# Performance work log

Hardware: AMD Instinct MI355X
Metric: run time of the kernel (lower is better)

## Reference

```python
import jax, jax.numpy as jnp
import numpy as np

B, P, H, W = 8, 128, 32, 32
NC = 4                 # num_classes = NUM_REL_GROUP + 1
DOBJ = 4424            # 2*DOBJ = 8848
CIN = 256
C = 128 + 8848         # 8976 GCN channel dim


def setup_inputs() -> dict:
    key = jax.random.key(0)
    ks = jax.random.split(key, 24)
    s = 0.02  # weight scale to keep activations moderate
    inp = {
        "x": jax.random.normal(ks[0], (B, CIN, H, W), jnp.float32),
        "rel_pair_idxs": jax.random.randint(ks[1], (B, P, 2), 0, 640, dtype=jnp.int32),
        "obj_rep": jax.random.normal(ks[2], (640, DOBJ), jnp.float32),
        # ADD_GCN params
        "fc_w": jax.random.normal(ks[3], (NC, CIN), jnp.float32) * s,
        "ct_w": jax.random.normal(ks[4], (128, CIN), jnp.float32) * s,
        "ct_b": jnp.zeros((128,), jnp.float32),
        # DynamicGraphConvolution params
        "A": jax.random.normal(ks[5], (NC, NC), jnp.float32) * 0.25,          # static_adj conv1d (no bias)
        "sw_w": jax.random.normal(ks[6], (C, C), jnp.float32) * s / np.sqrt(C) * 30,
        "sw_b": jnp.zeros((C,), jnp.float32),
        "cg_w": jax.random.normal(ks[7], (C, C), jnp.float32) * s / np.sqrt(C) * 30,
        "cg_b": jnp.zeros((C,), jnp.float32),
        "bn_g": jnp.ones((C,), jnp.float32),
        "bn_b": jnp.zeros((C,), jnp.float32),
        "bn_m": jnp.zeros((C,), jnp.float32),
        "bn_v": jnp.ones((C,), jnp.float32),
        "co_w": jax.random.normal(ks[8], (NC, 2 * C), jnp.float32) * s / np.sqrt(C) * 30,
        "co_b": jnp.zeros((NC,), jnp.float32),
        "dw_w": jax.random.normal(ks[9], (C, C), jnp.float32) * s / np.sqrt(C) * 30,
        "dw_b": jnp.zeros((C,), jnp.float32),
        "ll_w": jax.random.normal(ks[10], (NC, C), jnp.float32) * s / np.sqrt(C) * 30,
        "ll_b": jnp.zeros((NC,), jnp.float32),
        "mask_mat": jnp.eye(NC, dtype=jnp.float32),
    }
    return inp


def reference(x, rel_pair_idxs, obj_rep, fc_w, ct_w, ct_b, A, sw_w, sw_b,
              cg_w, cg_b, bn_g, bn_b, bn_m, bn_v, co_w, co_b, dw_w, dw_b,
              ll_w, ll_b, mask_mat):
    leaky = lambda t: jax.nn.leaky_relu(t, 0.2)
    b, cin, h, w = x.shape
    xr = x.reshape(b, cin, h * w)                                  # (B,256,HW)

    # forward_classification_sm: fc -> topk(1).mean == max over spatial
    y = jnp.einsum('oc,bcs->bos', fc_w, xr)                        # (B,NC,HW)
    out1 = y.max(-1)                                               # (B,NC)

    # forward_sam
    mask = jax.nn.sigmoid(y)                                       # (B,NC,HW)
    v = jnp.einsum('oc,bcs->bos', ct_w, xr) + ct_b[None, :, None]  # (B,128,HW)
    v = jnp.einsum('bcs,bns->bcn', v, mask)                        # (B,128,NC)

    # pairwise object features (gather), tiled over NC node slots
    o1 = obj_rep[rel_pair_idxs[..., 0]]                            # (B,P,DOBJ)
    o2 = obj_rep[rel_pair_idxs[..., 1]]
    pf = jnp.concatenate([o1, o2], -1)                             # (B,P,8848)
    p = pf.shape[1]
    pf = jnp.broadcast_to(pf[..., None], pf.shape + (NC,))         # (B,P,8848,NC)
    vb = jnp.broadcast_to(v[:, None], (b, p) + v.shape[1:])        # (B,P,128,NC)
    g = jnp.concatenate([pf, vb], 2).reshape(b * p, C, NC)         # (BP,C,NC)

    # --- DynamicGraphConvolution ---
    # static GCN: node-mix conv1d (no bias) + leaky, then channel 1x1 conv + leaky
    xs = leaky(jnp.einsum('nm,pcm->pcn', A, g))                    # (BP,C,NC)
    xs = leaky(jnp.einsum('oc,pcn->pon', sw_w, xs) + sw_b[None, :, None])
    hg = g + xs

    # dynamic adjacency
    glb = hg.mean(-1)                                              # (BP,C) gap
    glb = glb @ cg_w.T + cg_b                                      # conv_global (1x1)
    glb = (glb - bn_m) * jax.lax.rsqrt(bn_v + 1e-5) * bn_g + bn_b  # BN (eval)
    glb = leaky(glb)
    # conv_create_co_mat over cat([glb_expand, hg], ch) without materializing cat
    adj = jax.nn.sigmoid(
        jnp.einsum('oc,pc->po', co_w[:, :C], glb)[:, :, None]
        + jnp.einsum('oc,pcn->pon', co_w[:, C:], hg)
        + co_b[None, :, None])                                     # (BP,NC,NC)

    # dynamic GCN
    hd = leaky(jnp.einsum('pcn,pnm->pcm', hg, adj))
    z = leaky(jnp.einsum('oc,pcn->pon', dw_w, hd) + dw_b[None, :, None])  # (BP,C,NC)

    # head: last_linear + leaky, masked diagonal sum
    out2 = leaky(jnp.einsum('oc,pcn->pon', ll_w, z) + ll_b[None, :, None])  # (BP,NC,NC)
    out2 = (out2 * jax.lax.stop_gradient(mask_mat)).sum(-1)        # (BP,NC)

    o1b = jnp.broadcast_to(out1[:, None], (b, p, NC)).reshape(b * p, NC)
    return ((o1b + out2) * 0.5).reshape(b, p, NC)
```

## Files before the change

kernel.cpp:

```cpp
#include <hip/hip_runtime.h>
#include <stdint.h>

#define DEVI __device__ __forceinline__

typedef unsigned short u16;
typedef __bf16 bf16x8 __attribute__((ext_vector_type(8)));
typedef float f32x4 __attribute__((ext_vector_type(4)));
typedef u16 u16x8 __attribute__((ext_vector_type(8)));

DEVI u16 f2bf(float f){
  union { float f; unsigned u; } v; v.f = f;
  unsigned r = v.u + 0x7FFFu + ((v.u >> 16) & 1u);
  return (u16)(r >> 16);
}
DEVI float bf2f(u16 h){
  union { unsigned u; float f; } v; v.u = ((unsigned)h) << 16;
  return v.f;
}
DEVI float lky(float t){ return t > 0.f ? t : 0.2f * t; }

#define GLD16(gp, lp) __builtin_amdgcn_global_load_lds( \
    (const __attribute__((address_space(1))) void*)(gp), \
    (__attribute__((address_space(3))) void*)(lp), 16, 0, 0)


DEVI void stage_half(const u16* __restrict__ G, size_t grow0, int kcol, int Kp,
                     u16* lds, int t)
{
  #pragma unroll
  for (int j = 0; j < 2; ++j){
    const int off16 = j*512 + t;
    const int rl = off16 >> 3, sl = off16 & 7;
    const u16* gp = G + (grow0 + rl)*(size_t)Kp + kcol + ((sl ^ (rl & 7))*8);
    GLD16(gp, lds + off16*8);
  }
}

template<int RB, int RA>
DEVI void ph_reads(const u16* __restrict__ Ab, const u16* __restrict__ Bb,
                   bf16x8 (&afr)[4][2], bf16x8 (&bfr)[4][2],
                   int wr, int wc, int l4, int l15)
{
  if constexpr (RA >= 0){
    #pragma unroll
    for (int m = 0; m < 4; ++m){
      const int r = wr*128 + RA*64 + m*16 + l15;
      afr[m][0] = *(const bf16x8*)&Ab[r*64 + (((0+l4) ^ (r & 7))*8)];
      afr[m][1] = *(const bf16x8*)&Ab[r*64 + (((4+l4) ^ (r & 7))*8)];
    }
  }
  if constexpr (RB >= 0){
    #pragma unroll
    for (int nn = 0; nn < 2; ++nn){
      const int r = wc*64 + (RB+nn)*16 + l15;
      bfr[RB+nn][0] = *(const bf16x8*)&Bb[r*64 + (((0+l4) ^ (r & 7))*8)];
      bfr[RB+nn][1] = *(const bf16x8*)&Bb[r*64 + (((4+l4) ^ (r & 7))*8)];
    }
  }
}

template<int MH, int NH, int VM>
DEVI void ph_mfma(bf16x8 (&afr)[4][2], bf16x8 (&bfr)[4][2], f32x4 (&acc)[8][4])
{
  __builtin_amdgcn_s_barrier();
  asm volatile("s_waitcnt lgkmcnt(0)" ::: "memory");
  __builtin_amdgcn_sched_barrier(0);
  __builtin_amdgcn_s_setprio(1);
  #pragma unroll
  for (int m = 0; m < 4; ++m)
    #pragma unroll
    for (int nn = 0; nn < 2; ++nn)
      #pragma unroll
      for (int ks = 0; ks < 2; ++ks)
        acc[MH*4+m][NH+nn] = __builtin_amdgcn_mfma_f32_16x16x32_bf16(
            afr[m][ks], bfr[NH+nn][ks], acc[MH*4+m][NH+nn], 0, 0, 0);
  __builtin_amdgcn_s_setprio(0);
  if constexpr (VM == 4){
    __builtin_amdgcn_sched_barrier(0);
    asm volatile("s_waitcnt vmcnt(4)" ::: "memory");
  }
  __builtin_amdgcn_s_barrier();
}

template<int EPI>
__global__ __launch_bounds__(512, 2)
void gemm256(const u16* __restrict__ A, const u16* __restrict__ B,
             int Kp, int Nt, int Mreal, float* __restrict__ C, long long ldc,
             const float* __restrict__ bias, const float* __restrict__ scale,
             const float* __restrict__ off, const float* __restrict__ llw,
             float* __restrict__ oacc)
{
  __shared__ __align__(16) u16 As[2][16384];
  __shared__ __align__(16) u16 Bs[2][16384];
  const int t    = threadIdx.x;
  const int lane = t & 63;
  const int wid  = t >> 6;
  const int wr = wid >> 2, wc = wid & 3;
  const int l4 = lane >> 4, l15 = lane & 15;

  const int nwg = gridDim.x;
  const int xc = blockIdx.x & 7, pp = blockIdx.x >> 3;
  const int qq = nwg >> 3, rr = nwg & 7;
  const int wg = (xc < rr ? xc*(qq+1) : rr*(qq+1) + (xc-rr)*qq) + pp;
  const int mt = wg / Nt, nt = wg % Nt;

  const size_t am0 = (size_t)mt*256;
  const size_t bn0 = (size_t)nt*256;

  f32x4 acc[8][4];
  #pragma unroll
  for (int i = 0; i < 8; ++i)
    #pragma unroll
    for (int j = 0; j < 4; ++j) acc[i][j] = f32x4{0.f,0.f,0.f,0.f};
  bf16x8 afr[4][2], bfr[4][2];

  const int NT2 = Kp >> 6;
  const int NI  = NT2 >> 1;

  stage_half(A, am0+0,   0,  Kp, &As[0][0],    t);
  stage_half(A, am0+128, 0,  Kp, &As[0][8192], t);
  stage_half(B, bn0+0,   0,  Kp, &Bs[0][0],    t);
  stage_half(B, bn0+128, 0,  Kp, &Bs[0][8192], t);
  stage_half(B, bn0+0,   64, Kp, &Bs[1][0],    t);
  stage_half(B, bn0+128, 64, Kp, &Bs[1][8192], t);
  asm volatile("s_waitcnt vmcnt(4)" ::: "memory");
  __builtin_amdgcn_s_barrier();

  for (int i = 0; i < NI; ++i){
    const int k1  = 2*i + 1;
    const int ts0 = (2*i+2 < NT2) ? 2*i+2 : 2*i;
    const int ts1 = (2*i+3 < NT2) ? 2*i+3 : 2*i+1;
    ph_reads<0,0>(&As[0][0], &Bs[0][0], afr, bfr, wr, wc, l4, l15);
    stage_half(A, am0+0,   k1*64,  Kp, &As[1][0],    t);
    ph_mfma<0,0,-1>(afr, bfr, acc);
    ph_reads<2,-1>(&As[0][0], &Bs[0][0], afr, bfr, wr, wc, l4, l15);
    stage_half(A, am0+128, k1*64,  Kp, &As[1][8192], t);
    ph_mfma<0,2,-1>(afr, bfr, acc);
    ph_reads<-1,1>(&As[0][0], &Bs[0][0], afr, bfr, wr, wc, l4, l15);
    stage_half(B, bn0+0,   ts0*64, Kp, &Bs[0][0],    t);
    ph_mfma<1,2,-1>(afr, bfr, acc);
    stage_half(B, bn0+128, ts0*64, Kp, &Bs[0][8192], t);
    ph_mfma<1,0,4>(afr, bfr, acc);
    ph_reads<0,0>(&As[1][0], &Bs[1][0], afr, bfr, wr, wc, l4, l15);
    stage_half(A, am0+0,   ts0*64, Kp, &As[0][0],    t);
    ph_mfma<0,0,-1>(afr, bfr, acc);
    ph_reads<2,-1>(&As[1][0], &Bs[1][0], afr, bfr, wr, wc, l4, l15);
    stage_half(A, am0+128, ts0*64, Kp, &As[0][8192], t);
    ph_mfma<0,2,-1>(afr, bfr, acc);
    ph_reads<-1,1>(&As[1][0], &Bs[1][0], afr, bfr, wr, wc, l4, l15);
    stage_half(B, bn0+0,   ts1*64, Kp, &Bs[1][0],    t);
    ph_mfma<1,2,-1>(afr, bfr, acc);
    stage_half(B, bn0+128, ts1*64, Kp, &Bs[1][8192], t);
    ph_mfma<1,0,4>(afr, bfr, acc);
  }
  asm volatile("s_waitcnt vmcnt(0)" ::: "memory");

  const int ob0 = mt*256 + wr*128;
  const int nb0 = nt*256 + wc*64;

  if (EPI == 0){
    #pragma unroll
    for (int mi = 0; mi < 8; ++mi){
      const int ob = ob0 + mi*16 + l4*4;
      if (ob < Mreal){
        #pragma unroll
        for (int ni = 0; ni < 4; ++ni){
          const int n = nb0 + ni*16 + l15;
          *(f32x4*)&C[(size_t)n*ldc + ob] = acc[mi][ni];
        }
      }
    }
  } else if (EPI == 2){
    #pragma unroll
    for (int mi = 0; mi < 8; ++mi){
      const int ob = ob0 + mi*16 + l4*4;
      if (ob < Mreal){
        const float sc0=scale[ob],sc1=scale[ob+1],sc2=scale[ob+2],sc3=scale[ob+3];
        const float of0=off[ob],of1=off[ob+1],of2=off[ob+2],of3=off[ob+3];
        #pragma unroll
        for (int ni = 0; ni < 4; ++ni){
          const int n = nb0 + ni*16 + l15;
          f32x4 a = acc[mi][ni];
          f32x4 vv = { lky(a[0]*sc0+of0), lky(a[1]*sc1+of1),
                       lky(a[2]*sc2+of2), lky(a[3]*sc3+of3) };
          *(f32x4*)&C[(size_t)n*ldc + ob] = vv;
        }
      }
    }
  } else {
    #pragma unroll
    for (int ni = 0; ni < 4; ++ni){
      float s0=0.f, s1=0.f, s2=0.f, s3=0.f;
      #pragma unroll
      for (int mi = 0; mi < 8; ++mi){
        #pragma unroll
        for (int r = 0; r < 4; ++r){
          const int o = ob0 + mi*16 + l4*4 + r;
          if (o < Mreal){
            const float val = lky(acc[mi][ni][r] + bias[o]);
            s0 += llw[o]         * val;
            s1 += llw[8976 + o]  * val;
            s2 += llw[17952 + o] * val;
            s3 += llw[26928 + o] * val;
          }
        }
      }
      const int n = nb0 + ni*16 + l15;
      const int q = n >> 2, m = n & 3;
      float sv[4] = {s0,s1,s2,s3};
      #pragma unroll
      for (int o4 = 0; o4 < 4; ++o4){
        float tt = sv[o4];
        tt += __shfl_xor(tt, 16);
        tt += __shfl_xor(tt, 32);
        if (l4 == 0) atomicAdd(&oacc[(q*4 + o4)*4 + m], tt);
      }
    }
  }
}

template<int EPI>
__global__ __launch_bounds__(256)
void gemm_bf16(const u16* __restrict__ A, const u16* __restrict__ B,
               int Kp, int Nt, int Mreal, float* __restrict__ C, long long ldc,
               const float* __restrict__ bias)
{
  __shared__ __align__(16) u16 As[2][4096];
  __shared__ __align__(16) u16 Bs[2][4096];
  const int tid  = threadIdx.x;
  const int lane = tid & 63;
  const int wr   = (tid >> 6) >> 1, wc = (tid >> 6) & 1;
  const int l4   = lane >> 4, l15 = lane & 15;
  const int mt   = blockIdx.x / Nt, nt = blockIdx.x % Nt;

  const size_t arow = (size_t)(mt*128 + (tid>>2)) * Kp + (tid&3)*8;
  const size_t brow = (size_t)(nt*128 + (tid>>2)) * Kp + (tid&3)*8;
  const int    ldst = (tid>>2)*32 + (tid&3)*8;
  const size_t rowskip = (size_t)64 * Kp;

  f32x4 acc[4][4];
  #pragma unroll
  for (int i=0;i<4;i++)
    #pragma unroll
    for (int j=0;j<4;j++) acc[i][j] = f32x4{0.f,0.f,0.f,0.f};

  const int NT = Kp >> 5;
  {
    const u16* a0 = A + arow; const u16* b0 = B + brow;
    GLD16(a0,           &As[0][ldst]);
    GLD16(a0 + rowskip, &As[0][ldst + 2048]);
    GLD16(b0,           &Bs[0][ldst]);
    GLD16(b0 + rowskip, &Bs[0][ldst + 2048]);
  }
  __syncthreads();

  for (int kt=0; kt<NT; ++kt){
    const int cur = kt & 1;
    if (kt + 1 < NT){
      const u16* a0 = A + arow + (size_t)(kt+1)*32;
      const u16* b0 = B + brow + (size_t)(kt+1)*32;
      GLD16(a0,           &As[cur^1][ldst]);
      GLD16(a0 + rowskip, &As[cur^1][ldst + 2048]);
      GLD16(b0,           &Bs[cur^1][ldst]);
      GLD16(b0 + rowskip, &Bs[cur^1][ldst + 2048]);
    }
    bf16x8 af[4], bf[4];
    #pragma unroll
    for (int mi=0;mi<4;mi++)
      af[mi] = *(const bf16x8*)&As[cur][(wr*64 + mi*16 + l15)*32 + l4*8];
    #pragma unroll
    for (int ni=0;ni<4;ni++)
      bf[ni] = *(const bf16x8*)&Bs[cur][(wc*64 + ni*16 + l15)*32 + l4*8];
    #pragma unroll
    for (int mi=0;mi<4;mi++)
      #pragma unroll
      for (int ni=0;ni<4;ni++)
        acc[mi][ni] = __builtin_amdgcn_mfma_f32_16x16x32_bf16(af[mi], bf[ni], acc[mi][ni], 0, 0, 0);
    __syncthreads();
  }

  const int ob0 = mt*128 + wr*64;
  const int nb0 = nt*128 + wc*64;
  #pragma unroll
  for (int mi=0;mi<4;mi++)
    #pragma unroll
    for (int r=0;r<4;r++){
      const int o = ob0 + mi*16 + l4*4 + r;
      if (o < Mreal){
        const float bb = bias[o];
        #pragma unroll
        for (int ni=0;ni<4;ni++){
          const int n = nb0 + ni*16 + l15;
          C[(size_t)o*ldc + n] = acc[mi][ni][r] + bb;
        }
      }
    }
}

__global__ void k_cvt_pad(const float* __restrict__ src, int srows, int scols,
                          int lds_, int koff, u16* __restrict__ dst, int Kp)
{
  const int r = blockIdx.x;
  const int nch = Kp >> 3;
  for (int ch = threadIdx.x; ch < nch; ch += blockDim.x){
    const int k = ch*8;
    u16 o[8];
    if (r < srows){
      #pragma unroll
      for (int i=0;i<8;i++){
        const int kk = k + i;
        o[i] = (kk < scols) ? f2bf(src[(size_t)r*lds_ + koff + kk]) : (u16)0;
      }
    } else {
      #pragma unroll
      for (int i=0;i<8;i++) o[i] = 0;
    }
    u16x8 vv = { o[0],o[1],o[2],o[3],o[4],o[5],o[6],o[7] };
    *(u16x8*)&dst[(size_t)r*Kp + k] = vv;
  }
}

__global__ void k_cvt_obj(const float* __restrict__ obj, u16* __restrict__ dst)
{
  const int r = blockIdx.x;
  const int ab = (r >= 640);
  const float* src = obj + (size_t)(ab ? r-640 : r)*4424;
  for (int ch = threadIdx.x; ch < 560; ch += 256){
    const int k = ch*8;
    u16 o[8];
    #pragma unroll
    for (int i=0;i<8;i++){
      const int kk = k+i;
      float f = (kk < 4424) ? src[kk] : 0.f;
      if (ab) f = fabsf(f);
      o[i] = f2bf(f);
    }
    u16x8 vv = { o[0],o[1],o[2],o[3],o[4],o[5],o[6],o[7] };
    *(u16x8*)&dst[(size_t)r*4480 + k] = vv;
  }
}

__global__ void k_combine(const float* __restrict__ U, const int* __restrict__ rel,
                          float* __restrict__ P12)
{
  const int q = blockIdx.x;
  const int i1 = rel[q*2], i2 = rel[q*2+1];
  const float* u1  = U + (size_t)i1*17952;
  const float* u2  = U + (size_t)i2*17952 + 8976;
  const float* u1a = U + (size_t)(640+i1)*17952;
  const float* u2a = U + (size_t)(640+i2)*17952 + 8976;
  float* p1 = P12 + (size_t)q*8976;
  float* p2 = P12 + (size_t)(1024+q)*8976;
  for (int c = threadIdx.x*4; c < 8976; c += 1024){
    f32x4 a  = *(const f32x4*)&u1[c];
    f32x4 b  = *(const f32x4*)&u2[c];
    f32x4 aa = *(const f32x4*)&u1a[c];
    f32x4 bb = *(const f32x4*)&u2a[c];
    *(f32x4*)&p1[c] = a + b;
    *(f32x4*)&p2[c] = aa + bb;
  }
}

__global__ void k_xT(const float* __restrict__ x, u16* __restrict__ xT)
{
  __shared__ float t[32][33];
  const int bid = blockIdx.x;
  const int b = bid >> 8; const int cs = (bid >> 5) & 7; const int ss = bid & 31;
  const int tx = threadIdx.x & 31, ty = threadIdx.x >> 5;
  #pragma unroll
  for (int i=0;i<4;i++){
    const int r = ty + i*8;
    t[r][tx] = x[((size_t)(b*256 + cs*32 + r))*1024 + ss*32 + tx];
  }
  __syncthreads();
  #pragma unroll
  for (int i=0;i<4;i++){
    const int r = ty + i*8;
    xT[((size_t)(b*1024 + ss*32 + r))*256 + cs*32 + tx] = f2bf(t[tx][r]);
  }
}

__global__ void k_ymask(const float* __restrict__ x, const float* __restrict__ fcw,
                        float* __restrict__ y, float* __restrict__ mask)
{
  __shared__ float fc[1024];
  const int b = blockIdx.x >> 2, st = blockIdx.x & 3;
  for (int i=threadIdx.x; i<1024; i+=256) fc[i] = fcw[i];
  __syncthreads();
  const int s = st*256 + threadIdx.x;
  float a0=0,a1=0,a2=0,a3=0;
  for (int c=0;c<256;c++){
    const float xv = x[((size_t)(b*256+c))*1024 + s];
    a0 += fc[c]*xv; a1 += fc[256+c]*xv; a2 += fc[512+c]*xv; a3 += fc[768+c]*xv;
  }
  const size_t base = (size_t)(b*4)*1024 + s;
  y[base]        = a0; mask[base]        = 1.f/(1.f+expf(-a0));
  y[base+1024]   = a1; mask[base+1024]   = 1.f/(1.f+expf(-a1));
  y[base+2048]   = a2; mask[base+2048]   = 1.f/(1.f+expf(-a2));
  y[base+3072]   = a3; mask[base+3072]   = 1.f/(1.f+expf(-a3));
}

__global__ void k_out1(const float* __restrict__ y, float* __restrict__ out1){
  const int bn = blockIdx.x;
  float m = -3.4e38f;
  for (int s=threadIdx.x; s<1024; s+=256) m = fmaxf(m, y[(size_t)bn*1024+s]);
  for (int o=32;o;o>>=1) m = fmaxf(m, __shfl_xor(m,o));
  __shared__ float red[4];
  if ((threadIdx.x&63)==0) red[threadIdx.x>>6] = m;
  __syncthreads();
  if (threadIdx.x==0) out1[bn] = fmaxf(fmaxf(red[0],red[1]),fmaxf(red[2],red[3]));
}

__global__ void k_v(const float* __restrict__ vpreT, const float* __restrict__ mask,
                    float* __restrict__ v){
  const int b = blockIdx.x >> 7, j = blockIdx.x & 127;
  float a[4]={0,0,0,0};
  for (int s=threadIdx.x; s<1024; s+=256){
    const float pv = vpreT[(size_t)j*8192 + b*1024 + s];
    #pragma unroll
    for (int m=0;m<4;m++) a[m] += pv * mask[((size_t)(b*4+m))*1024 + s];
  }
  __shared__ float red[4][5];
  #pragma unroll
  for (int m=0;m<4;m++){
    float t=a[m];
    for (int o=32;o;o>>=1) t += __shfl_xor(t,o);
    if ((threadIdx.x&63)==0) red[m][threadIdx.x>>6]=t;
  }
  __syncthreads();
  if (threadIdx.x<4)
    v[(size_t)(b*128+j)*4 + threadIdx.x] =
      red[threadIdx.x][0]+red[threadIdx.x][1]+red[threadIdx.x][2]+red[threadIdx.x][3];
}

__global__ void k_lv(const float* __restrict__ Am, const float* __restrict__ v,
                     float* __restrict__ lv){
  const int idx = blockIdx.x*256 + threadIdx.x;
  if (idx < 1024){
    #pragma unroll
    for (int n=0;n<4;n++){
      float s=0;
      #pragma unroll
      for (int m=0;m<4;m++) s += Am[n*4+m]*v[idx*4+m];
      lv[idx*4+n] = lky(s);
    }
  }
}

__global__ void k_sV(const float* __restrict__ sw, const float* __restrict__ lv,
                     float* __restrict__ sV){
  __shared__ float l[4096];
  for (int i=threadIdx.x; i<4096; i+=256) l[i]=lv[i];
  __syncthreads();
  const int o = blockIdx.x*256 + threadIdx.x;
  if (o >= 8976) return;
  float acc[8][4] = {};
  const float* row = sw + (size_t)o*8976 + 8848;
  for (int j=0;j<128;j++){
    const float wv = row[j];
    #pragma unroll
    for (int b=0;b<8;b++){
      const float* lb = &l[(b*128+j)*4];
      #pragma unroll
      for (int n=0;n<4;n++) acc[b][n] += wv*lb[n];
    }
  }
  #pragma unroll
  for (int b=0;b<8;b++){
    f32x4 vv = {acc[b][0],acc[b][1],acc[b][2],acc[b][3]};
    *(f32x4*)&sV[((size_t)b*8976 + o)*4] = vv;
  }
}

__global__ void k_so(const float* __restrict__ cgb, const float* __restrict__ g,
                     const float* __restrict__ b2, const float* __restrict__ m,
                     const float* __restrict__ vvar, float* __restrict__ so){
  const int o = blockIdx.x*256+threadIdx.x;
  if (o<8976){
    const float sc = g[o]*rsqrtf(vvar[o]+1e-5f);
    so[o]=sc; so[8976+o] = (cgb[o]-m[o])*sc + b2[o];
  }
}

__global__ void k_glb_t2(const float* __restrict__ P12, const float* __restrict__ obj,
                         const int* __restrict__ rel,
                         const float* __restrict__ sV, const float* __restrict__ swb,
                         const float* __restrict__ v, const float* __restrict__ Am,
                         const float* __restrict__ cow, u16* __restrict__ glbB,
                         float* __restrict__ t2)
{
  const int q = blockIdx.x; const int b = q >> 7;
  const int i1 = rel[q*2], i2 = rel[q*2+1];
  const float* o1 = obj + (size_t)i1*4424;
  const float* o2 = obj + (size_t)i2*4424;
  float rA[4], aA[4];
  #pragma unroll
  for (int n=0;n<4;n++){
    const float s = Am[n*4]+Am[n*4+1]+Am[n*4+2]+Am[n*4+3];
    rA[n]=0.6f*s; aA[n]=0.4f*fabsf(s);
  }
  float t2a[16] = {};
  for (int c = threadIdx.x; c < 9216; c += 256){
    if (c < 8976){
      const float p1 = P12[(size_t)q*8976 + c];
      const float p2 = P12[(size_t)(1024+q)*8976 + c];
      const f32x4 sv = *(const f32x4*)&sV[((size_t)b*8976 + c)*4];
      const float sb = swb[c];
      const float gs = (c < 4424) ? o1[c] : (c < 8848) ? o2[c-4424] : 0.f;
      float hg[4]; float sum = 0.f;
      #pragma unroll
      for (int n=0;n<4;n++){
        const float xs2 = lky(rA[n]*p1 + aA[n]*p2 + sv[n] + sb);
        const float g = (c < 8848) ? gs : v[((size_t)b*128 + (c-8848))*4 + n];
        hg[n] = g + xs2; sum += hg[n];
      }
      glbB[(size_t)q*9216 + c] = f2bf(0.25f*sum);
      #pragma unroll
      for (int o4=0;o4<4;o4++){
        const float cw = cow[(size_t)o4*17952 + 8976 + c];
        #pragma unroll
        for (int n=0;n<4;n++) t2a[o4*4+n] += cw*hg[n];
      }
    } else {
      glbB[(size_t)q*9216 + c] = 0;
    }
  }
  __shared__ float red[16][5];
  #pragma unroll
  for (int i=0;i<16;i++){
    float t = t2a[i];
    for (int o=32;o;o>>=1) t += __shfl_xor(t,o);
    if ((threadIdx.x&63)==0) red[i][threadIdx.x>>6]=t;
  }
  __syncthreads();
  if (threadIdx.x < 16)
    t2[q*16+threadIdx.x] = red[threadIdx.x][0]+red[threadIdx.x][1]
                          +red[threadIdx.x][2]+red[threadIdx.x][3];
}

__global__ void k_adj(const float* __restrict__ glb2, const float* __restrict__ cow,
                      const float* __restrict__ t2, const float* __restrict__ cob,
                      float* __restrict__ adj)
{
  const int q = blockIdx.x;
  float a[4]={0,0,0,0};
  for (int c=threadIdx.x; c<8976; c+=256){
    const float g = glb2[(size_t)q*8976+c];
    #pragma unroll
    for (int o=0;o<4;o++) a[o] += cow[(size_t)o*17952 + c]*g;
  }
  __shared__ float red[4][5]; __shared__ float co1[4];
  #pragma unroll
  for (int i=0;i<4;i++){
    float t=a[i]; for (int o=32;o;o>>=1) t += __shfl_xor(t,o);
    if ((threadIdx.x&63)==0) red[i][threadIdx.x>>6]=t;
  }
  __syncthreads();
  if (threadIdx.x<4)
    co1[threadIdx.x]=red[threadIdx.x][0]+red[threadIdx.x][1]+red[threadIdx.x][2]+red[threadIdx.x][3];
  __syncthreads();
  if (threadIdx.x<16){
    const int a_=threadIdx.x>>2, m=threadIdx.x&3;
    const float t = co1[a_] + t2[q*16 + a_*4 + m] + cob[a_];
    adj[q*16 + a_*4 + m] = 1.f/(1.f+expf(-t));
  }
}

__global__ void k_hd(const float* __restrict__ P12, const float* __restrict__ obj,
                     const int* __restrict__ rel,
                     const float* __restrict__ sV, const float* __restrict__ swb,
                     const float* __restrict__ v, const float* __restrict__ Am,
                     const float* __restrict__ adj, u16* __restrict__ hdb)
{
  const int q = blockIdx.x; const int b = q>>7;
  const int i1 = rel[q*2], i2 = rel[q*2+1];
  const float* o1 = obj + (size_t)i1*4424;
  const float* o2 = obj + (size_t)i2*4424;
  float rA[4], aA[4];
  #pragma unroll
  for (int n=0;n<4;n++){
    const float s = Am[n*4]+Am[n*4+1]+Am[n*4+2]+Am[n*4+3];
    rA[n]=0.6f*s; aA[n]=0.4f*fabsf(s);
  }
  __shared__ float aj[16];
  if (threadIdx.x<16) aj[threadIdx.x] = adj[q*16+threadIdx.x];
  __syncthreads();
  float ajr[16];
  #pragma unroll
  for (int i=0;i<16;i++) ajr[i]=aj[i];
  for (int c=threadIdx.x; c<9216; c+=256){
    if (c<8976){
      const float p1 = P12[(size_t)q*8976 + c];
      const float p2 = P12[(size_t)(1024+q)*8976 + c];
      const f32x4 sv = *(const f32x4*)&sV[((size_t)b*8976 + c)*4];
      const float sb = swb[c];
      const float gs = (c < 4424) ? o1[c] : (c < 8848) ? o2[c-4424] : 0.f;
      float hg[4];
      #pragma unroll
      for (int n=0;n<4;n++){
        const float xs2 = lky(rA[n]*p1 + aA[n]*p2 + sv[n] + sb);
        const float g = (c < 8848) ? gs : v[((size_t)b*128 + (c-8848))*4 + n];
        hg[n] = g + xs2;
      }
      #pragma unroll
      for (int m=0;m<4;m++){
        const float hv = lky(hg[0]*ajr[m] + hg[1]*ajr[4+m] + hg[2]*ajr[8+m] + hg[3]*ajr[12+m]);
        hdb[((size_t)(q*4+m))*9216 + c] = f2bf(hv);
      }
    } else {
      #pragma unroll
      for (int m=0;m<4;m++) hdb[((size_t)(q*4+m))*9216 + c] = 0;
    }
  }
}

__global__ void k_final(const float* __restrict__ o2f, const float* __restrict__ out1,
                        const float* __restrict__ llb, const float* __restrict__ mm,
                        float* __restrict__ out)
{
  const int idx = blockIdx.x*256+threadIdx.x;
  if (idx < 4096){
    const int q = idx>>2, o = idx&3, b = q>>7;
    float s=0.f;
    #pragma unroll
    for (int m=0;m<4;m++) s += lky(o2f[(q*4+o)*4+m] + llb[o]) * mm[o*4+m];
    out[idx] = 0.5f*(out1[b*4+o] + s);
  }
}

extern "C" void kernel_launch(void* const* d_in, const int* in_sizes, int n_in,
                              void* d_out, int out_size, void* d_ws, size_t ws_size,
                              hipStream_t stream)
{
  const float* x    = (const float*)d_in[0];
  const int*   rel  = (const int*)d_in[1];
  const float* obj  = (const float*)d_in[2];
  const float* fcw  = (const float*)d_in[3];
  const float* ctw  = (const float*)d_in[4];
  const float* ctb  = (const float*)d_in[5];
  const float* Am   = (const float*)d_in[6];
  const float* sww  = (const float*)d_in[7];
  const float* swb  = (const float*)d_in[8];
  const float* cgw  = (const float*)d_in[9];
  const float* cgb  = (const float*)d_in[10];
  const float* bng  = (const float*)d_in[11];
  const float* bnb  = (const float*)d_in[12];
  const float* bnm  = (const float*)d_in[13];
  const float* bnv  = (const float*)d_in[14];
  const float* cow  = (const float*)d_in[15];
  const float* cob  = (const float*)d_in[16];
  const float* dww  = (const float*)d_in[17];
  const float* dwb  = (const float*)d_in[18];
  const float* llw  = (const float*)d_in[19];
  const float* llb  = (const float*)d_in[20];
  const float* mm   = (const float*)d_in[21];
  float* out = (float*)d_out;
  (void)in_sizes; (void)n_in; (void)out_size; (void)ws_size;

  char* ws = (char*)d_ws;
  size_t off = 0;
  auto alloc = [&](size_t bytes)->char*{
    char* p = ws + off; off = (off + bytes + 255) & ~(size_t)255; return p;
  };
  u16*   Wb    = (u16*)  alloc((size_t)9216*9216*2);
  char*  UG    = alloc((size_t)94371840);
  float* U     = (float*)UG;
  u16*   glbB  = (u16*)  UG;
  u16*   hdb   = (u16*)  (UG + (size_t)18874368);
  u16*   objB  = (u16*)  alloc((size_t)1280*4480*2);
  float* P12   = (float*)alloc((size_t)2048*8976*4);
  float* glb2  = (float*)alloc((size_t)1024*8976*4);
  u16*   xT    = (u16*)  alloc((size_t)8192*256*2);
  u16*   ctwb  = (u16*)  alloc((size_t)128*256*2);
  float* y     = (float*)alloc((size_t)32768*4);
  float* mask  = (float*)alloc((size_t)32768*4);
  float* out1  = (float*)alloc((size_t)32*4);
  float* vpreT = (float*)alloc((size_t)128*8192*4);
  float* v     = (float*)alloc((size_t)4096*4);
  float* lv    = (float*)alloc((size_t)4096*4);
  float* sV    = (float*)alloc((size_t)287232*4);
  float* so    = (float*)alloc((size_t)2*8976*4);
  float* t2    = (float*)alloc((size_t)16384*4);
  float* adj   = (float*)alloc((size_t)16384*4);
  float* o2f   = (float*)alloc((size_t)16384*4);

  k_xT<<<dim3(2048), dim3(256), 0, stream>>>(x, xT);
  k_cvt_pad<<<dim3(128), dim3(256), 0, stream>>>(ctw, 128, 256, 256, 0, ctwb, 256);
  k_ymask<<<dim3(32), dim3(256), 0, stream>>>(x, fcw, y, mask);
  k_out1<<<dim3(32), dim3(256), 0, stream>>>(y, out1);
  gemm_bf16<1><<<dim3(64), dim3(256), 0, stream>>>(
      ctwb, xT, 256, 64, 128, vpreT, (long long)8192, ctb);
  k_v<<<dim3(1024), dim3(256), 0, stream>>>(vpreT, mask, v);

  k_cvt_obj<<<dim3(1280), dim3(256), 0, stream>>>(obj, objB);
  k_cvt_pad<<<dim3(8976), dim3(256), 0, stream>>>(sww, 8976, 4424, 8976, 0, Wb, 4480);
  k_cvt_pad<<<dim3(9200), dim3(256), 0, stream>>>(sww, 8976, 4424, 8976, 4424,
                                                  Wb + (size_t)8976*4480, 4480);
  gemm256<0><<<dim3(71*5), dim3(512), 0, stream>>>(
      Wb, objB, 4480, 5, 17952, U, (long long)17952,
      nullptr, nullptr, nullptr, nullptr, nullptr);
  k_combine<<<dim3(1024), dim3(256), 0, stream>>>(U, rel, P12);

  k_lv<<<dim3(4), dim3(256), 0, stream>>>(Am, v, lv);
  k_sV<<<dim3(36), dim3(256), 0, stream>>>(sww, lv, sV);
  k_glb_t2<<<dim3(1024), dim3(256), 0, stream>>>(P12, obj, rel, sV, swb, v, Am,
                                                 cow, glbB, t2);

  k_cvt_pad<<<dim3(9216), dim3(256), 0, stream>>>(cgw, 8976, 8976, 8976, 0, Wb, 9216);
  k_so<<<dim3(36), dim3(256), 0, stream>>>(cgb, bng, bnb, bnm, bnv, so);
  gemm256<2><<<dim3(36*4), dim3(512), 0, stream>>>(
      Wb, glbB, 9216, 4, 8976, glb2, (long long)8976,
      nullptr, so, so + 8976, nullptr, nullptr);

  k_adj<<<dim3(1024), dim3(256), 0, stream>>>(glb2, cow, t2, cob, adj);
  k_cvt_pad<<<dim3(9216), dim3(256), 0, stream>>>(dww, 8976, 8976, 8976, 0, Wb, 9216);
  k_hd<<<dim3(1024), dim3(256), 0, stream>>>(P12, obj, rel, sV, swb, v, Am, adj, hdb);

  hipMemsetAsync(o2f, 0, (size_t)16384*4, stream);
  gemm256<3><<<dim3(36*16), dim3(512), 0, stream>>>(
      Wb, hdb, 9216, 16, 8976, nullptr, 0, dwb,
      nullptr, nullptr, llw, o2f);

  k_final<<<dim3(16), dim3(256), 0, stream>>>(o2f, out1, llb, mm, out);
}
```

Baseline: 2.165 ms.

## Fuse fp32-to-bf16 weight conversion into GEMM A-operand loads

Removes the separate k_cvt_pad passes that wrote the large weight matrices to a bf16 workspace. The GEMM now loads fp32 weights directly into registers, converts them to bf16 and writes them into swizzled LDS inside the pipelined main loop, with bounds masking and stacked-row handling for the sw_w split. The K padding for the glb and hd operands shrinks from 9216 to 9088. This trades a full extra read and write of each weight matrix for more register pressure, conversion ALU work inside the loop and a more complex wait and barrier schedule.

```diff
diff --git a/kernel.cpp b/kernel.cpp
--- a/kernel.cpp
+++ b/kernel.cpp
@@ -7,6 +7,7 @@
 typedef __bf16 bf16x8 __attribute__((ext_vector_type(8)));
 typedef float f32x4 __attribute__((ext_vector_type(4)));
 typedef u16 u16x8 __attribute__((ext_vector_type(8)));
+typedef u16 u16x4 __attribute__((ext_vector_type(4)));
 
 DEVI u16 f2bf(float f){
   union { float f; unsigned u; } v; v.f = f;
@@ -24,43 +25,8 @@
     (__attribute__((address_space(3))) void*)(lp), 16, 0, 0)
 
 
-DEVI void stage_half(const u16* __restrict__ G, size_t grow0, int kcol, int Kp,
-                     u16* lds, int t)
-{
-  #pragma unroll
-  for (int j = 0; j < 2; ++j){
-    const int off16 = j*512 + t;
-    const int rl = off16 >> 3, sl = off16 & 7;
-    const u16* gp = G + (grow0 + rl)*(size_t)Kp + kcol + ((sl ^ (rl & 7))*8);
-    GLD16(gp, lds + off16*8);
-  }
-}
-
-template<int RB, int RA>
-DEVI void ph_reads(const u16* __restrict__ Ab, const u16* __restrict__ Bb,
-                   bf16x8 (&afr)[4][2], bf16x8 (&bfr)[4][2],
-                   int wr, int wc, int l4, int l15)
-{
-  if constexpr (RA >= 0){
-    #pragma unroll
-    for (int m = 0; m < 4; ++m){
-      const int r = wr*128 + RA*64 + m*16 + l15;
-      afr[m][0] = *(const bf16x8*)&Ab[r*64 + (((0+l4) ^ (r & 7))*8)];
-      afr[m][1] = *(const bf16x8*)&Ab[r*64 + (((4+l4) ^ (r & 7))*8)];
-    }
-  }
-  if constexpr (RB >= 0){
-    #pragma unroll
-    for (int nn = 0; nn < 2; ++nn){
-      const int r = wc*64 + (RB+nn)*16 + l15;
-      bfr[RB+nn][0] = *(const bf16x8*)&Bb[r*64 + (((0+l4) ^ (r & 7))*8)];
-      bfr[RB+nn][1] = *(const bf16x8*)&Bb[r*64 + (((4+l4) ^ (r & 7))*8)];
-    }
-  }
-}
-
-template<int MH, int NH, int VM>
-DEVI void ph_mfma(bf16x8 (&afr)[4][2], bf16x8 (&bfr)[4][2], f32x4 (&acc)[8][4])
+template<int VM>
+DEVI void PH(bf16x8 (&afr)[4], bf16x8 (&bfr)[4], f32x4 (&acc)[8][4], int H)
 {
   __builtin_amdgcn_s_barrier();
   asm volatile("s_waitcnt lgkmcnt(0)" ::: "memory");
@@ -69,26 +35,28 @@
   #pragma unroll
   for (int m = 0; m < 4; ++m)
     #pragma unroll
-    for (int nn = 0; nn < 2; ++nn)
-      #pragma unroll
-      for (int ks = 0; ks < 2; ++ks)
-        acc[MH*4+m][NH+nn] = __builtin_amdgcn_mfma_f32_16x16x32_bf16(
-            afr[m][ks], bfr[NH+nn][ks], acc[MH*4+m][NH+nn], 0, 0, 0);
+    for (int n = 0; n < 4; ++n)
+      acc[H*4+m][n] = __builtin_amdgcn_mfma_f32_16x16x32_bf16(
+          afr[m], bfr[n], acc[H*4+m][n], 0, 0, 0);
   __builtin_amdgcn_s_setprio(0);
-  if constexpr (VM == 4){
+  if constexpr (VM == 10){
     __builtin_amdgcn_sched_barrier(0);
-    asm volatile("s_waitcnt vmcnt(4)" ::: "memory");
+    asm volatile("s_waitcnt vmcnt(10)" ::: "memory");
+  } else if constexpr (VM == 12){
+    __builtin_amdgcn_sched_barrier(0);
+    asm volatile("s_waitcnt vmcnt(12)" ::: "memory");
   }
   __builtin_amdgcn_s_barrier();
 }
 
-template<int EPI>
+template<int EPI, int STACKED>
 __global__ __launch_bounds__(512, 2)
-void gemm256(const u16* __restrict__ A, const u16* __restrict__ B,
-             int Kp, int Nt, int Mreal, float* __restrict__ C, long long ldc,
-             const float* __restrict__ bias, const float* __restrict__ scale,
-             const float* __restrict__ off, const float* __restrict__ llw,
-             float* __restrict__ oacc)
+void gemmF(const float* __restrict__ A, const u16* __restrict__ B,
+           int Astride, int Kreal, int Kp, int Mrows, int Nt, int Mreal,
+           float* __restrict__ C, long long ldc,
+           const float* __restrict__ bias, const float* __restrict__ scale,
+           const float* __restrict__ off, const float* __restrict__ llw,
+           float* __restrict__ oacc)
 {
   __shared__ __align__(16) u16 As[2][16384];
   __shared__ __align__(16) u16 Bs[2][16384];
@@ -104,56 +72,117 @@
   const int wg = (xc < rr ? xc*(qq+1) : rr*(qq+1) + (xc-rr)*qq) + pp;
   const int mt = wg / Nt, nt = wg % Nt;
 
-  const size_t am0 = (size_t)mt*256;
-  const size_t bn0 = (size_t)nt*256;
+  const int am0 = mt*256;
+  const int bn0 = nt*256;
 
   f32x4 acc[8][4];
   #pragma unroll
   for (int i = 0; i < 8; ++i)
     #pragma unroll
     for (int j = 0; j < 4; ++j) acc[i][j] = f32x4{0.f,0.f,0.f,0.f};
-  bf16x8 afr[4][2], bfr[4][2];
+  bf16x8 afr[4], bfr[4];
+  f32x4 ra[8];
 
   const int NT2 = Kp >> 6;
   const int NI  = NT2 >> 1;
 
-  stage_half(A, am0+0,   0,  Kp, &As[0][0],    t);
-  stage_half(A, am0+128, 0,  Kp, &As[0][8192], t);
-  stage_half(B, bn0+0,   0,  Kp, &Bs[0][0],    t);
-  stage_half(B, bn0+128, 0,  Kp, &Bs[0][8192], t);
-  stage_half(B, bn0+0,   64, Kp, &Bs[1][0],    t);
-  stage_half(B, bn0+128, 64, Kp, &Bs[1][8192], t);
-  asm volatile("s_waitcnt vmcnt(4)" ::: "memory");
+  auto BSTAGE = [&](int tile, int buf, int h){
+    const int kc = tile*64;
+    u16* lbase = (buf ? &Bs[1][0] : &Bs[0][0]) + h*8192;
+    #pragma unroll
+    for (int j = 0; j < 2; ++j){
+      const int u = j*512 + t;
+      const int rl = u >> 3, sl = u & 7;
+      const u16* gp = B + (size_t)(bn0 + h*128 + rl)*Kp + kc + ((sl ^ (rl & 7))*8);
+      GLD16(gp, lbase + u*8);
+    }
+  };
+  auto ALOAD = [&](int tile){
+    const int kc = tile*64;
+    #pragma unroll
+    for (int j = 0; j < 8; ++j){
+      const int h = j >> 2;
+      const int u = (j & 3)*512 + t;
+      const int row = am0 + h*128 + (u >> 4);
+      const int col = kc + (u & 15)*4;
+      int ro = row, ko = 0;
+      if (STACKED){ if (row >= 8976){ ro = row - 8976; ko = 4424; } }
+      const bool ok = (row < Mrows) && (col < Kreal);
+      const float* p = A + (size_t)(ok ? ro : 0)*Astride + ko + (ok ? col : 0);
+      f32x4 v = __builtin_nontemporal_load((const f32x4*)p);
+      ra[j] = ok ? v : f32x4{0.f,0.f,0.f,0.f};
+    }
+  };
+  auto AWRITE_H = [&](int buf, int h){
+    u16* lb = buf ? &As[1][0] : &As[0][0];
+    #pragma unroll
+    for (int jj = 0; jj < 4; ++jj){
+      const int j = h*4 + jj;
+      const int u = jj*512 + t;
+      const int rl = h*128 + (u >> 4);
+      const int cu = u & 15, koct = cu >> 1, hu = cu & 1;
+      f32x4 v = ra[j];
+      u16x4 w = { f2bf(v[0]), f2bf(v[1]), f2bf(v[2]), f2bf(v[3]) };
+      *(u16x4*)&lb[rl*64 + ((koct ^ (rl & 7))*8) + hu*4] = w;
+    }
+  };
+  auto RDA = [&](int buf, int h, int ks){
+    const u16* lb = buf ? &As[1][0] : &As[0][0];
+    #pragma unroll
+    for (int m = 0; m < 4; ++m){
+      const int r = wr*128 + h*64 + m*16 + l15;
+      afr[m] = *(const bf16x8*)&lb[r*64 + (((ks*4 + l4) ^ (r & 7))*8)];
+    }
+  };
+  auto RDB = [&](int buf, int ks){
+    const u16* lb = buf ? &Bs[1][0] : &Bs[0][0];
+    #pragma unroll
+    for (int n = 0; n < 4; ++n){
+      const int r = wc*64 + n*16 + l15;
+      bfr[n] = *(const bf16x8*)&lb[r*64 + (((ks*4 + l4) ^ (r & 7))*8)];
+    }
+  };
+  #define FENCE asm volatile("" ::: "memory")
+
+  ALOAD(0);                 FENCE;
+  BSTAGE(0,0,0); BSTAGE(0,0,1);  FENCE;
+  AWRITE_H(0,0); AWRITE_H(0,1);  FENCE;
+  BSTAGE(1,1,0); BSTAGE(1,1,1);  FENCE;
+  ALOAD(1);                 FENCE;
+  asm volatile("s_waitcnt vmcnt(12)" ::: "memory");
+  asm volatile("s_waitcnt lgkmcnt(0)" ::: "memory");
   __builtin_amdgcn_s_barrier();
 
   for (int i = 0; i < NI; ++i){
-    const int k1  = 2*i + 1;
-    const int ts0 = (2*i+2 < NT2) ? 2*i+2 : 2*i;
-    const int ts1 = (2*i+3 < NT2) ? 2*i+3 : 2*i+1;
-    ph_reads<0,0>(&As[0][0], &Bs[0][0], afr, bfr, wr, wc, l4, l15);
-    stage_half(A, am0+0,   k1*64,  Kp, &As[1][0],    t);
-    ph_mfma<0,0,-1>(afr, bfr, acc);
-    ph_reads<2,-1>(&As[0][0], &Bs[0][0], afr, bfr, wr, wc, l4, l15);
-    stage_half(A, am0+128, k1*64,  Kp, &As[1][8192], t);
-    ph_mfma<0,2,-1>(afr, bfr, acc);
-    ph_reads<-1,1>(&As[0][0], &Bs[0][0], afr, bfr, wr, wc, l4, l15);
-    stage_half(B, bn0+0,   ts0*64, Kp, &Bs[0][0],    t);
-    ph_mfma<1,2,-1>(afr, bfr, acc);
-    stage_half(B, bn0+128, ts0*64, Kp, &Bs[0][8192], t);
-    ph_mfma<1,0,4>(afr, bfr, acc);
-    ph_reads<0,0>(&As[1][0], &Bs[1][0], afr, bfr, wr, wc, l4, l15);
-    stage_half(A, am0+0,   ts0*64, Kp, &As[0][0],    t);
-    ph_mfma<0,0,-1>(afr, bfr, acc);
-    ph_reads<2,-1>(&As[1][0], &Bs[1][0], afr, bfr, wr, wc, l4, l15);
-    stage_half(A, am0+128, ts0*64, Kp, &As[0][8192], t);
-    ph_mfma<0,2,-1>(afr, bfr, acc);
-    ph_reads<-1,1>(&As[1][0], &Bs[1][0], afr, bfr, wr, wc, l4, l15);
-    stage_half(B, bn0+0,   ts1*64, Kp, &Bs[1][0],    t);
-    ph_mfma<1,2,-1>(afr, bfr, acc);
-    stage_half(B, bn0+128, ts1*64, Kp, &Bs[1][8192], t);
-    ph_mfma<1,0,4>(afr, bfr, acc);
-  }
-  asm volatile("s_waitcnt vmcnt(0)" ::: "memory");
+    const int ta = (2*i+2 < NT2) ? 2*i+2 : NT2-1;
+    const int tb = (2*i+3 < NT2) ? 2*i+3 : NT2-1;
+    AWRITE_H(1,0);
+    RDA(0,0,0); RDB(0,0);
+    PH<-1>(afr, bfr, acc, 0);
+    AWRITE_H(1,1);
+    RDA(0,1,0);
+    PH<-1>(afr, bfr, acc, 1);
+    RDA(0,0,1); RDB(0,1);
+    ALOAD(ta);
+    PH<-1>(afr, bfr, acc, 0);
+    RDA(0,1,1);
+    BSTAGE(ta,0,0);
+    PH<10>(afr, bfr, acc, 1);
+    AWRITE_H(0,0);
+    RDA(1,0,0); RDB(1,0);
+    BSTAGE(ta,0,1);
+    PH<-1>(afr, bfr, acc, 0);
+    AWRITE_H(0,1);
+    RDA(1,1,0);
+    PH<-1>(afr, bfr, acc, 1);
+    RDA(1,0,1); RDB(1,1);
+    ALOAD(tb);
+    PH<-1>(afr, bfr, acc, 0);
+    RDA(1,1,1);
+    BSTAGE(tb,1,0); BSTAGE(tb,1,1);
+    PH<12>(afr, bfr, acc, 1);
+  }
+  asm volatile("s_waitcnt vmcnt(0) lgkmcnt(0)" ::: "memory");
 
   const int ob0 = mt*256 + wr*128;
   const int nb0 = nt*256 + wc*64;
@@ -219,9 +248,8 @@
   }
 }
 
-template<int EPI>
 __global__ __launch_bounds__(256)
-void gemm_bf16(const u16* __restrict__ A, const u16* __restrict__ B,
+void gemm_vpre(const u16* __restrict__ A, const u16* __restrict__ B,
                int Kp, int Nt, int Mreal, float* __restrict__ C, long long ldc,
                const float* __restrict__ bias)
 {
@@ -500,7 +528,7 @@
     rA[n]=0.6f*s; aA[n]=0.4f*fabsf(s);
   }
   float t2a[16] = {};
-  for (int c = threadIdx.x; c < 9216; c += 256){
+  for (int c = threadIdx.x; c < 9088; c += 256){
     if (c < 8976){
       const float p1 = P12[(size_t)q*8976 + c];
       const float p2 = P12[(size_t)(1024+q)*8976 + c];
@@ -514,7 +542,7 @@
         const float g = (c < 8848) ? gs : v[((size_t)b*128 + (c-8848))*4 + n];
         hg[n] = g + xs2; sum += hg[n];
       }
-      glbB[(size_t)q*9216 + c] = f2bf(0.25f*sum);
+      glbB[(size_t)q*9088 + c] = f2bf(0.25f*sum);
       #pragma unroll
       for (int o4=0;o4<4;o4++){
         const float cw = cow[(size_t)o4*17952 + 8976 + c];
@@ -522,7 +550,7 @@
         for (int n=0;n<4;n++) t2a[o4*4+n] += cw*hg[n];
       }
     } else {
-      glbB[(size_t)q*9216 + c] = 0;
+      glbB[(size_t)q*9088 + c] = 0;
     }
   }
   __shared__ float red[16][5];
@@ -588,7 +616,7 @@
   float ajr[16];
   #pragma unroll
   for (int i=0;i<16;i++) ajr[i]=aj[i];
-  for (int c=threadIdx.x; c<9216; c+=256){
+  for (int c=threadIdx.x; c<9088; c+=256){
     if (c<8976){
       const float p1 = P12[(size_t)q*8976 + c];
       const float p2 = P12[(size_t)(1024+q)*8976 + c];
@@ -605,11 +633,11 @@
       #pragma unroll
       for (int m=0;m<4;m++){
         const float hv = lky(hg[0]*ajr[m] + hg[1]*ajr[4+m] + hg[2]*ajr[8+m] + hg[3]*ajr[12+m]);
-        hdb[((size_t)(q*4+m))*9216 + c] = f2bf(hv);
+        hdb[((size_t)(q*4+m))*9088 + c] = f2bf(hv);
       }
     } else {
       #pragma unroll
-      for (int m=0;m<4;m++) hdb[((size_t)(q*4+m))*9216 + c] = 0;
+      for (int m=0;m<4;m++) hdb[((size_t)(q*4+m))*9088 + c] = 0;
     }
   }
 }
@@ -662,11 +690,10 @@
   auto alloc = [&](size_t bytes)->char*{
     char* p = ws + off; off = (off + bytes + 255) & ~(size_t)255; return p;
   };
-  u16*   Wb    = (u16*)  alloc((size_t)9216*9216*2);
   char*  UG    = alloc((size_t)94371840);
   float* U     = (float*)UG;
   u16*   glbB  = (u16*)  UG;
-  u16*   hdb   = (u16*)  (UG + (size_t)18874368);
+  u16*   hdb   = (u16*)  (UG + (size_t)1024*9088*2);
   u16*   objB  = (u16*)  alloc((size_t)1280*4480*2);
   float* P12   = (float*)alloc((size_t)2048*8976*4);
   float* glb2  = (float*)alloc((size_t)1024*8976*4);
@@ -688,16 +715,13 @@
   k_cvt_pad<<<dim3(128), dim3(256), 0, stream>>>(ctw, 128, 256, 256, 0, ctwb, 256);
   k_ymask<<<dim3(32), dim3(256), 0, stream>>>(x, fcw, y, mask);
   k_out1<<<dim3(32), dim3(256), 0, stream>>>(y, out1);
-  gemm_bf16<1><<<dim3(64), dim3(256), 0, stream>>>(
+  gemm_vpre<<<dim3(64), dim3(256), 0, stream>>>(
       ctwb, xT, 256, 64, 128, vpreT, (long long)8192, ctb);
   k_v<<<dim3(1024), dim3(256), 0, stream>>>(vpreT, mask, v);
 
   k_cvt_obj<<<dim3(1280), dim3(256), 0, stream>>>(obj, objB);
-  k_cvt_pad<<<dim3(8976), dim3(256), 0, stream>>>(sww, 8976, 4424, 8976, 0, Wb, 4480);
-  k_cvt_pad<<<dim3(9200), dim3(256), 0, stream>>>(sww, 8976, 4424, 8976, 4424,
-                                                  Wb + (size_t)8976*4480, 4480);
-  gemm256<0><<<dim3(71*5), dim3(512), 0, stream>>>(
-      Wb, objB, 4480, 5, 17952, U, (long long)17952,
+  gemmF<0,1><<<dim3(71*5), dim3(512), 0, stream>>>(
+      sww, objB, 8976, 4424, 4480, 17952, 5, 17952, U, (long long)17952,
       nullptr, nullptr, nullptr, nullptr, nullptr);
   k_combine<<<dim3(1024), dim3(256), 0, stream>>>(U, rel, P12);
 
@@ -706,20 +730,18 @@
   k_glb_t2<<<dim3(1024), dim3(256), 0, stream>>>(P12, obj, rel, sV, swb, v, Am,
                                                  cow, glbB, t2);
 
-  k_cvt_pad<<<dim3(9216), dim3(256), 0, stream>>>(cgw, 8976, 8976, 8976, 0, Wb, 9216);
   k_so<<<dim3(36), dim3(256), 0, stream>>>(cgb, bng, bnb, bnm, bnv, so);
-  gemm256<2><<<dim3(36*4), dim3(512), 0, stream>>>(
-      Wb, glbB, 9216, 4, 8976, glb2, (long long)8976,
+  gemmF<2,0><<<dim3(36*4), dim3(512), 0, stream>>>(
+      cgw, glbB, 8976, 8976, 9088, 8976, 4, 8976, glb2, (long long)8976,
       nullptr, so, so + 8976, nullptr, nullptr);
 
   k_adj<<<dim3(1024), dim3(256), 0, stream>>>(glb2, cow, t2, cob, adj);
-  k_cvt_pad<<<dim3(9216), dim3(256), 0, stream>>>(dww, 8976, 8976, 8976, 0, Wb, 9216);
   k_hd<<<dim3(1024), dim3(256), 0, stream>>>(P12, obj, rel, sV, swb, v, Am, adj, hdb);
 
   hipMemsetAsync(o2f, 0, (size_t)16384*4, stream);
-  gemm256<3><<<dim3(36*16), dim3(512), 0, stream>>>(
-      Wb, hdb, 9216, 16, 8976, nullptr, 0, dwb,
-      nullptr, nullptr, llw, o2f);
+  gemmF<3,0><<<dim3(36*16), dim3(512), 0, stream>>>(
+      dww, hdb, 8976, 8976, 9088, 8976, 16, 8976, nullptr, 0,
+      dwb, nullptr, nullptr, llw, o2f);
 
   k_final<<<dim3(16), dim3(256), 0, stream>>>(o2f, out1, llb, mm, out);
 }
```

Result: slower. 4.118 ms (+90.2%).

## Fuse pair-combine into consumers, shrink K padding, add strip tile ordering

Applied to the files above, without the earlier changes.

Removes the k_combine kernel and the P12 intermediate: k_glb_t2 and k_hd now gather the two U rows per pair and add them inline. The K padding for the 8976-dim GEMMs drops from 9216 to 9088, so the weight conversion and the GEMM main loops do less padded work. gemm256 gains an SN parameter that groups N-tiles into strips to improve L2 reuse, and the dw GEMM uses strips of 8. The intent is to cut memory traffic and one launch. In exchange U is read twice with scattered rows, and the 9088 padding must stay compatible with the 128-wide K step.

```diff
diff --git a/kernel.cpp b/kernel.cpp
--- a/kernel.cpp
+++ b/kernel.cpp
@@ -85,7 +85,7 @@
 template<int EPI>
 __global__ __launch_bounds__(512, 2)
 void gemm256(const u16* __restrict__ A, const u16* __restrict__ B,
-             int Kp, int Nt, int Mreal, float* __restrict__ C, long long ldc,
+             int Kp, int Nt, int SN, int Mreal, float* __restrict__ C, long long ldc,
              const float* __restrict__ bias, const float* __restrict__ scale,
              const float* __restrict__ off, const float* __restrict__ llw,
              float* __restrict__ oacc)
@@ -102,7 +102,9 @@
   const int xc = blockIdx.x & 7, pp = blockIdx.x >> 3;
   const int qq = nwg >> 3, rr = nwg & 7;
   const int wg = (xc < rr ? xc*(qq+1) : rr*(qq+1) + (xc-rr)*qq) + pp;
-  const int mt = wg / Nt, nt = wg % Nt;
+  const int strip_sz = (nwg / Nt) * SN;
+  const int strip = wg / strip_sz, srem = wg % strip_sz;
+  const int mt = srem / SN, nt = strip*SN + srem % SN;
 
   const size_t am0 = (size_t)mt*256;
   const size_t bn0 = (size_t)nt*256;
@@ -219,9 +221,8 @@
   }
 }
 
-template<int EPI>
 __global__ __launch_bounds__(256)
-void gemm_bf16(const u16* __restrict__ A, const u16* __restrict__ B,
+void gemm_vpre(const u16* __restrict__ A, const u16* __restrict__ B,
                int Kp, int Nt, int Mreal, float* __restrict__ C, long long ldc,
                const float* __restrict__ bias)
 {
@@ -340,27 +341,6 @@
   }
 }
 
-__global__ void k_combine(const float* __restrict__ U, const int* __restrict__ rel,
-                          float* __restrict__ P12)
-{
-  const int q = blockIdx.x;
-  const int i1 = rel[q*2], i2 = rel[q*2+1];
-  const float* u1  = U + (size_t)i1*17952;
-  const float* u2  = U + (size_t)i2*17952 + 8976;
-  const float* u1a = U + (size_t)(640+i1)*17952;
-  const float* u2a = U + (size_t)(640+i2)*17952 + 8976;
-  float* p1 = P12 + (size_t)q*8976;
-  float* p2 = P12 + (size_t)(1024+q)*8976;
-  for (int c = threadIdx.x*4; c < 8976; c += 1024){
-    f32x4 a  = *(const f32x4*)&u1[c];
-    f32x4 b  = *(const f32x4*)&u2[c];
-    f32x4 aa = *(const f32x4*)&u1a[c];
-    f32x4 bb = *(const f32x4*)&u2a[c];
-    *(f32x4*)&p1[c] = a + b;
-    *(f32x4*)&p2[c] = aa + bb;
-  }
-}
-
 __global__ void k_xT(const float* __restrict__ x, u16* __restrict__ xT)
 {
   __shared__ float t[32][33];
@@ -482,7 +462,7 @@
   }
 }
 
-__global__ void k_glb_t2(const float* __restrict__ P12, const float* __restrict__ obj,
+__global__ void k_glb_t2(const float* __restrict__ U, const float* __restrict__ obj,
                          const int* __restrict__ rel,
                          const float* __restrict__ sV, const float* __restrict__ swb,
                          const float* __restrict__ v, const float* __restrict__ Am,
@@ -491,6 +471,10 @@
 {
   const int q = blockIdx.x; const int b = q >> 7;
   const int i1 = rel[q*2], i2 = rel[q*2+1];
+  const float* u1  = U + (size_t)i1*17952;
+  const float* u2  = U + (size_t)i2*17952 + 8976;
+  const float* u1a = U + (size_t)(640+i1)*17952;
+  const float* u2a = U + (size_t)(640+i2)*17952 + 8976;
   const float* o1 = obj + (size_t)i1*4424;
   const float* o2 = obj + (size_t)i2*4424;
   float rA[4], aA[4];
@@ -500,10 +484,10 @@
     rA[n]=0.6f*s; aA[n]=0.4f*fabsf(s);
   }
   float t2a[16] = {};
-  for (int c = threadIdx.x; c < 9216; c += 256){
+  for (int c = threadIdx.x; c < 9088; c += 256){
     if (c < 8976){
-      const float p1 = P12[(size_t)q*8976 + c];
-      const float p2 = P12[(size_t)(1024+q)*8976 + c];
+      const float p1 = u1[c] + u2[c];
+      const float p2 = u1a[c] + u2a[c];
       const f32x4 sv = *(const f32x4*)&sV[((size_t)b*8976 + c)*4];
       const float sb = swb[c];
       const float gs = (c < 4424) ? o1[c] : (c < 8848) ? o2[c-4424] : 0.f;
@@ -514,7 +498,7 @@
         const float g = (c < 8848) ? gs : v[((size_t)b*128 + (c-8848))*4 + n];
         hg[n] = g + xs2; sum += hg[n];
       }
-      glbB[(size_t)q*9216 + c] = f2bf(0.25f*sum);
+      glbB[(size_t)q*9088 + c] = f2bf(0.25f*sum);
       #pragma unroll
       for (int o4=0;o4<4;o4++){
         const float cw = cow[(size_t)o4*17952 + 8976 + c];
@@ -522,7 +506,7 @@
         for (int n=0;n<4;n++) t2a[o4*4+n] += cw*hg[n];
       }
     } else {
-      glbB[(size_t)q*9216 + c] = 0;
+      glbB[(size_t)q*9088 + c] = 0;
     }
   }
   __shared__ float red[16][5];
@@ -566,7 +550,7 @@
   }
 }
 
-__global__ void k_hd(const float* __restrict__ P12, const float* __restrict__ obj,
+__global__ void k_hd(const float* __restrict__ U, const float* __restrict__ obj,
                      const int* __restrict__ rel,
                      const float* __restrict__ sV, const float* __restrict__ swb,
                      const float* __restrict__ v, const float* __restrict__ Am,
@@ -574,6 +558,10 @@
 {
   const int q = blockIdx.x; const int b = q>>7;
   const int i1 = rel[q*2], i2 = rel[q*2+1];
+  const float* u1  = U + (size_t)i1*17952;
+  const float* u2  = U + (size_t)i2*17952 + 8976;
+  const float* u1a = U + (size_t)(640+i1)*17952;
+  const float* u2a = U + (size_t)(640+i2)*17952 + 8976;
   const float* o1 = obj + (size_t)i1*4424;
   const float* o2 = obj + (size_t)i2*4424;
   float rA[4], aA[4];
@@ -588,10 +576,10 @@
   float ajr[16];
   #pragma unroll
   for (int i=0;i<16;i++) ajr[i]=aj[i];
-  for (int c=threadIdx.x; c<9216; c+=256){
+  for (int c=threadIdx.x; c<9088; c+=256){
     if (c<8976){
-      const float p1 = P12[(size_t)q*8976 + c];
-      const float p2 = P12[(size_t)(1024+q)*8976 + c];
+      const float p1 = u1[c] + u2[c];
+      const float p2 = u1a[c] + u2a[c];
       const f32x4 sv = *(const f32x4*)&sV[((size_t)b*8976 + c)*4];
       const float sb = swb[c];
       const float gs = (c < 4424) ? o1[c] : (c < 8848) ? o2[c-4424] : 0.f;
@@ -605,11 +593,11 @@
       #pragma unroll
       for (int m=0;m<4;m++){
         const float hv = lky(hg[0]*ajr[m] + hg[1]*ajr[4+m] + hg[2]*ajr[8+m] + hg[3]*ajr[12+m]);
-        hdb[((size_t)(q*4+m))*9216 + c] = f2bf(hv);
+        hdb[((size_t)(q*4+m))*9088 + c] = f2bf(hv);
       }
     } else {
       #pragma unroll
-      for (int m=0;m<4;m++) hdb[((size_t)(q*4+m))*9216 + c] = 0;
+      for (int m=0;m<4;m++) hdb[((size_t)(q*4+m))*9088 + c] = 0;
     }
   }
 }
@@ -662,13 +650,11 @@
   auto alloc = [&](size_t bytes)->char*{
     char* p = ws + off; off = (off + bytes + 255) & ~(size_t)255; return p;
   };
-  u16*   Wb    = (u16*)  alloc((size_t)9216*9216*2);
-  char*  UG    = alloc((size_t)94371840);
-  float* U     = (float*)UG;
-  u16*   glbB  = (u16*)  UG;
-  u16*   hdb   = (u16*)  (UG + (size_t)18874368);
+  u16*   Wb    = (u16*)  alloc((size_t)9216*9088*2);
+  float* U     = (float*)alloc((size_t)1280*17952*4);
+  u16*   glbB  = (u16*)  alloc((size_t)1024*9088*2);
+  u16*   hdb   = (u16*)  alloc((size_t)4096*9088*2);
   u16*   objB  = (u16*)  alloc((size_t)1280*4480*2);
-  float* P12   = (float*)alloc((size_t)2048*8976*4);
   float* glb2  = (float*)alloc((size_t)1024*8976*4);
   u16*   xT    = (u16*)  alloc((size_t)8192*256*2);
   u16*   ctwb  = (u16*)  alloc((size_t)128*256*2);
@@ -688,7 +674,7 @@
   k_cvt_pad<<<dim3(128), dim3(256), 0, stream>>>(ctw, 128, 256, 256, 0, ctwb, 256);
   k_ymask<<<dim3(32), dim3(256), 0, stream>>>(x, fcw, y, mask);
   k_out1<<<dim3(32), dim3(256), 0, stream>>>(y, out1);
-  gemm_bf16<1><<<dim3(64), dim3(256), 0, stream>>>(
+  gemm_vpre<<<dim3(64), dim3(256), 0, stream>>>(
       ctwb, xT, 256, 64, 128, vpreT, (long long)8192, ctb);
   k_v<<<dim3(1024), dim3(256), 0, stream>>>(vpreT, mask, v);
 
@@ -697,28 +683,27 @@
   k_cvt_pad<<<dim3(9200), dim3(256), 0, stream>>>(sww, 8976, 4424, 8976, 4424,
                                                   Wb + (size_t)8976*4480, 4480);
   gemm256<0><<<dim3(71*5), dim3(512), 0, stream>>>(
-      Wb, objB, 4480, 5, 17952, U, (long long)17952,
+      Wb, objB, 4480, 5, 5, 17952, U, (long long)17952,
       nullptr, nullptr, nullptr, nullptr, nullptr);
-  k_combine<<<dim3(1024), dim3(256), 0, stream>>>(U, rel, P12);
 
   k_lv<<<dim3(4), dim3(256), 0, stream>>>(Am, v, lv);
   k_sV<<<dim3(36), dim3(256), 0, stream>>>(sww, lv, sV);
-  k_glb_t2<<<dim3(1024), dim3(256), 0, stream>>>(P12, obj, rel, sV, swb, v, Am,
+  k_glb_t2<<<dim3(1024), dim3(256), 0, stream>>>(U, obj, rel, sV, swb, v, Am,
                                                  cow, glbB, t2);
 
-  k_cvt_pad<<<dim3(9216), dim3(256), 0, stream>>>(cgw, 8976, 8976, 8976, 0, Wb, 9216);
+  k_cvt_pad<<<dim3(9216), dim3(256), 0, stream>>>(cgw, 8976, 8976, 8976, 0, Wb, 9088);
   k_so<<<dim3(36), dim3(256), 0, stream>>>(cgb, bng, bnb, bnm, bnv, so);
   gemm256<2><<<dim3(36*4), dim3(512), 0, stream>>>(
-      Wb, glbB, 9216, 4, 8976, glb2, (long long)8976,
+      Wb, glbB, 9088, 4, 4, 8976, glb2, (long long)8976,
       nullptr, so, so + 8976, nullptr, nullptr);
 
   k_adj<<<dim3(1024), dim3(256), 0, stream>>>(glb2, cow, t2, cob, adj);
-  k_cvt_pad<<<dim3(9216), dim3(256), 0, stream>>>(dww, 8976, 8976, 8976, 0, Wb, 9216);
-  k_hd<<<dim3(1024), dim3(256), 0, stream>>>(P12, obj, rel, sV, swb, v, Am, adj, hdb);
+  k_cvt_pad<<<dim3(9216), dim3(256), 0, stream>>>(dww, 8976, 8976, 8976, 0, Wb, 9088);
+  k_hd<<<dim3(1024), dim3(256), 0, stream>>>(U, obj, rel, sV, swb, v, Am, adj, hdb);
 
   hipMemsetAsync(o2f, 0, (size_t)16384*4, stream);
   gemm256<3><<<dim3(36*16), dim3(512), 0, stream>>>(
-      Wb, hdb, 9216, 16, 8976, nullptr, 0, dwb,
+      Wb, hdb, 9088, 16, 8, 8976, nullptr, 0, dwb,
       nullptr, nullptr, llw, o2f);
 
   k_final<<<dim3(16), dim3(256), 0, stream>>>(o2f, out1, llb, mm, out);
```

Result: faster. 2.112 ms (-2.4%).
